# Kernel tuning notes

Measured on AMD Instinct MI355X. Metric: run time of the kernel, lower is better.

Reference implementation:

```python
import jax, jax.numpy as jnp
import numpy as np


def _next_power2(n: int) -> int:
    return 1 << (n - 1).bit_length()


def setup_inputs() -> dict:
    key = jax.random.key(0)
    k1, k2, k3 = jax.random.split(key, 3)
    N, C, W = 32, 8, 65536
    F, WW = 16, 64
    x = jax.random.normal(k1, (N, C, W), dtype=jnp.float32)
    w = jax.random.normal(k2, (F, C, WW), dtype=jnp.float32)
    b = jax.random.normal(k3, (F,), dtype=jnp.float32)
    return {"x": x, "w": w, "b": b}


def reference(x, w, b):
    # FFT-based 1D cross-correlation (valid mode), no spectral compression
    # (preserve_energy_rate=index_back=out_size=padding=None).
    N, C, W = x.shape
    F, _, WW = w.shape
    out_W = W - WW + 1
    fftsize = _next_power2(W + WW - 1)
    Xf = jnp.fft.rfft(x, fftsize)                     # (N, C, Fr) complex
    Wf = jnp.fft.rfft(w, fftsize)                     # (F, C, Fr) complex
    # correlation = irfft(X * conj(W)); sum over channels C
    prod = jnp.einsum("ncf,kcf->nkf", Xf, jnp.conj(Wf))  # (N, F, Fr)
    out = jnp.fft.irfft(prod, fftsize)[..., :out_W]      # (N, F, out_W)
    # Original code adds bias[ff] inside the channel loop -> bias added C times.
    return out + (C * b)[None, :, None]
```

## Files before the change

kernel.cpp:

```cpp
#include <hip/hip_runtime.h>
#include <stdint.h>

typedef _Float16 half8 __attribute__((ext_vector_type(8)));
typedef __fp16 fp16x2 __attribute__((ext_vector_type(2)));
typedef float f32x4 __attribute__((ext_vector_type(4)));
typedef float f32x2 __attribute__((ext_vector_type(2)));
typedef uint32_t u32x2 __attribute__((ext_vector_type(2)));

#define N_ 32
#define C_ 8
#define W_ 65536
#define F_ 16
#define OW_ 65473
#define K_ 512
#define TILE_T 1024
#define XS 1152
#define SCP 140
#define SCW 4480

__device__ __forceinline__ uint32_t funnel16(uint32_t hi, uint32_t lo) {
  return (uint32_t)((((uint64_t)hi << 32) | (uint64_t)lo) >> 16);
}

__device__ __forceinline__ uint32_t pk(float a, float b) {
  union { fp16x2 h; uint32_t u; } cv;
  cv.h = __builtin_amdgcn_cvt_pkrtz(a, b);
  return cv.u;
}

__device__ __forceinline__ uint32_t wswz(uint32_t e) {
  uint32_t ch = e >> 3;
  ch ^= (ch >> 6) & 7u;
  return (ch << 4) | ((e & 7u) << 1);
}

__device__ __forceinline__ f32x4 ldx(const float* p) {
  return *reinterpret_cast<const f32x4*>(p);
}

template<bool TAIL>
__device__ __forceinline__ void block_job(const float* __restrict__ x,
                                          const float* __restrict__ w,
                                          const float* __restrict__ b,
                                          float* __restrict__ out,
                                          char* smem, int n, int t0) {
  _Float16* wl = reinterpret_cast<_Float16*>(smem);
  _Float16* xb = reinterpret_cast<_Float16*>(smem + 16384);

  const int tid  = threadIdx.x;
  const int lane = tid & 63;
  const int wv   = tid >> 6;
  const int c15  = lane & 15;
  const int g    = lane >> 4;

  const float* xn = x + (size_t)n * (C_ * W_);

  #pragma unroll
  for (int j = 0; j < 4; ++j) {
    int e = (tid + 512 * j) * 4;
    f32x4 v = ldx(w + e);
    u32x2 p; p[0] = pk(v[0], v[1]); p[1] = pk(v[2], v[3]);
    *reinterpret_cast<u32x2*>(reinterpret_cast<char*>(wl) + wswz((uint32_t)e)) = p;
  }

  #pragma unroll
  for (int j = 0; j < 5; ++j) {
    int u = tid + 512 * j;
    if (j == 4 && u >= 2176) break;
    int ch = u / 272;
    int pos = (u - ch * 272) * 4;
    int gi = t0 + pos;
    f32x4 v;
    if (TAIL) v = (gi < W_) ? ldx(xn + (size_t)ch * W_ + gi) : (f32x4){0.f,0.f,0.f,0.f};
    else      v = ldx(xn + (size_t)ch * W_ + gi);
    u32x2 p; p[0] = pk(v[0], v[1]); p[1] = pk(v[2], v[3]);
    *reinterpret_cast<u32x2*>(reinterpret_cast<char*>(xb) + (size_t)(ch * XS + pos) * 2u) = p;
  }

  const f32x4 bv = *reinterpret_cast<const f32x4*>(b + 4 * g);

  __syncthreads();

  const int tlw = wv << 7;

  f32x4 acc[8];
  #pragma unroll
  for (int r = 0; r < 8; ++r) acc[r] = (f32x4){0.f, 0.f, 0.f, 0.f};

  union Win { half8 h[2]; uint32_t d[8]; };

  #pragma unroll
  for (int s = 0; s < 16; ++s) {
    const uint32_t we = (uint32_t)(c15 * K_ + 32 * s + 8 * g);
    const half8 wf = *reinterpret_cast<const half8*>(
                         reinterpret_cast<const char*>(wl) + wswz(we));
    const int c  = s >> 1;
    const int jb = (s & 1) * 32;
    const int A0 = tlw + 8 * c15 + jb + 8 * g;
    Win win;
    win.h[0] = *reinterpret_cast<const half8*>(xb + c * XS + A0);
    win.h[1] = *reinterpret_cast<const half8*>(xb + c * XS + A0 + 8);
    #pragma unroll
    for (int r = 0; r < 8; ++r) {
      union { uint32_t d[4]; half8 h; } fr;
      const int m = r >> 1;
      if ((r & 1) == 0) {
        fr.d[0] = win.d[m];     fr.d[1] = win.d[m + 1];
        fr.d[2] = win.d[m + 2]; fr.d[3] = win.d[m + 3];
      } else {
        fr.d[0] = funnel16(win.d[m + 1], win.d[m]);
        fr.d[1] = funnel16(win.d[m + 2], win.d[m + 1]);
        fr.d[2] = funnel16(win.d[m + 3], win.d[m + 2]);
        fr.d[3] = funnel16(win.d[m + 4], win.d[m + 3]);
      }
      acc[r] = __builtin_amdgcn_mfma_f32_16x16x32_f16(wf, fr.h, acc[r], 0, 0, 0);
    }
  }

  __syncthreads();

  float* sc = reinterpret_cast<float*>(smem + (size_t)wv * SCW);
  float* outn = out + (size_t)n * F_ * OW_;
  const int Tw  = t0 + tlw;
  const int flr = lane >> 3;
  const int k   = lane & 7;

  #pragma unroll
  for (int cb = 0; cb < 2; ++cb) {
    const int qb = 2 * cb;
    #pragma unroll
    for (int dq = 0; dq < 2; ++dq) {
      const int q  = qb + dq;
      const int fl = 2 * g + dq;
      const float bias = 8.0f * bv[q];
      f32x4 lo = { acc[0][q] + bias, acc[1][q] + bias,
                   acc[2][q] + bias, acc[3][q] + bias };
      f32x4 hi = { acc[4][q] + bias, acc[5][q] + bias,
                   acc[6][q] + bias, acc[7][q] + bias };
      *reinterpret_cast<f32x4*>(sc + fl * SCP + 8 * c15)     = lo;
      *reinterpret_cast<f32x4*>(sc + fl * SCP + 8 * c15 + 4) = hi;
    }
    const int f  = 4 * (flr >> 1) + qb + (flr & 1);
    const int tf = (16 - f) & 15;
    float* row = outn + (size_t)f * OW_ + Tw;
    #pragma unroll
    for (int j = 0; j < 7; ++j) {
      const int t = tf + 2 * k + 16 * j;
      f32x2 v = { sc[flr * SCP + t], sc[flr * SCP + t + 1] };
      if (!TAIL || Tw + t + 2 <= OW_) {
        *reinterpret_cast<f32x2*>(row + t) = v;
      } else {
        if (Tw + t     < OW_) row[t]     = v[0];
        if (Tw + t + 1 < OW_) row[t + 1] = v[1];
      }
    }
    #pragma unroll
    for (int e2 = 0; e2 < 2; ++e2) {
      const int e = k + 8 * e2;
      const int t = (e < tf) ? e : 112 + e;
      if (!TAIL || Tw + t < OW_) row[t] = sc[flr * SCP + t];
    }
  }
}

__global__ __launch_bounds__(512, 6)
void corr1d(const float* __restrict__ x, const float* __restrict__ w,
            const float* __restrict__ b, float* __restrict__ out) {
  __shared__ __align__(16) char smem[35840];

  const int n  = blockIdx.x >> 6;
  const int tt = blockIdx.x & 63;
  const int t0 = tt * TILE_T;

  if (tt < 63) block_job<false>(x, w, b, out, smem, n, t0);
  else         block_job<true >(x, w, b, out, smem, n, t0);
}

extern "C" void kernel_launch(void* const* d_in, const int* in_sizes, int n_in,
                              void* d_out, int out_size, void* d_ws, size_t ws_size,
                              hipStream_t stream) {
  (void)in_sizes; (void)n_in; (void)out_size; (void)d_ws; (void)ws_size;
  const float* x = (const float*)d_in[0];
  const float* w = (const float*)d_in[1];
  const float* b = (const float*)d_in[2];
  float* out = (float*)d_out;
  corr1d<<<dim3(32 * 64), dim3(512), 0, stream>>>(x, w, b, out);
}
```

Baseline: 50.68 us.

## Keep filter fragments in registers and loop blocks over multiple smaller tiles

Loads the fp16 weight fragments straight from global into registers once per block instead of staging them through swizzled shared memory. Blocks shrink to 256 threads and each handles four consecutive 512-sample tiles in a loop, so the weight load and conversion is amortised and shared memory use drops to about 18 KB. The cost is more registers per thread (16 half8 fragments) and an extra barrier per tile. Within each block, tile loads and compute are serialised with no prefetch, and the grid shrinks to 1024 blocks.

```diff
diff --git a/kernel.cpp b/kernel.cpp
--- a/kernel.cpp
+++ b/kernel.cpp
@@ -13,8 +13,9 @@
 #define F_ 16
 #define OW_ 65473
 #define K_ 512
-#define TILE_T 1024
-#define XS 1152
+#define TILE_T 512
+#define NT_ 4
+#define XS 576
 #define SCP 140
 #define SCW 4480
 
@@ -28,152 +29,154 @@
   return cv.u;
 }
 
-__device__ __forceinline__ uint32_t wswz(uint32_t e) {
-  uint32_t ch = e >> 3;
-  ch ^= (ch >> 6) & 7u;
-  return (ch << 4) | ((e & 7u) << 1);
-}
-
 __device__ __forceinline__ f32x4 ldx(const float* p) {
   return *reinterpret_cast<const f32x4*>(p);
 }
 
-template<bool TAIL>
+template<bool TAILB>
 __device__ __forceinline__ void block_job(const float* __restrict__ x,
                                           const float* __restrict__ w,
                                           const float* __restrict__ b,
                                           float* __restrict__ out,
-                                          char* smem, int n, int t0) {
-  _Float16* wl = reinterpret_cast<_Float16*>(smem);
-  _Float16* xb = reinterpret_cast<_Float16*>(smem + 16384);
+                                          char* smem, int n, int tb0) {
+  _Float16* xb = reinterpret_cast<_Float16*>(smem);
 
   const int tid  = threadIdx.x;
   const int lane = tid & 63;
   const int wv   = tid >> 6;
   const int c15  = lane & 15;
   const int g    = lane >> 4;
+  const int tlw  = wv << 7;
 
   const float* xn = x + (size_t)n * (C_ * W_);
+  float* outn = out + (size_t)n * F_ * OW_;
 
-  #pragma unroll
-  for (int j = 0; j < 4; ++j) {
-    int e = (tid + 512 * j) * 4;
-    f32x4 v = ldx(w + e);
-    u32x2 p; p[0] = pk(v[0], v[1]); p[1] = pk(v[2], v[3]);
-    *reinterpret_cast<u32x2*>(reinterpret_cast<char*>(wl) + wswz((uint32_t)e)) = p;
+  half8 wf[16];
+  {
+    const float* wrow = w + c15 * K_ + 8 * g;
+    #pragma unroll
+    for (int s = 0; s < 16; ++s) {
+      f32x4 a = ldx(wrow + 32 * s);
+      f32x4 c = ldx(wrow + 32 * s + 4);
+      union { uint32_t d[4]; half8 h; } u;
+      u.d[0] = pk(a[0], a[1]); u.d[1] = pk(a[2], a[3]);
+      u.d[2] = pk(c[0], c[1]); u.d[3] = pk(c[2], c[3]);
+      wf[s] = u.h;
+    }
   }
-
-  #pragma unroll
-  for (int j = 0; j < 5; ++j) {
-    int u = tid + 512 * j;
-    if (j == 4 && u >= 2176) break;
-    int ch = u / 272;
-    int pos = (u - ch * 272) * 4;
-    int gi = t0 + pos;
-    f32x4 v;
-    if (TAIL) v = (gi < W_) ? ldx(xn + (size_t)ch * W_ + gi) : (f32x4){0.f,0.f,0.f,0.f};
-    else      v = ldx(xn + (size_t)ch * W_ + gi);
-    u32x2 p; p[0] = pk(v[0], v[1]); p[1] = pk(v[2], v[3]);
-    *reinterpret_cast<u32x2*>(reinterpret_cast<char*>(xb) + (size_t)(ch * XS + pos) * 2u) = p;
-  }
-
   const f32x4 bv = *reinterpret_cast<const f32x4*>(b + 4 * g);
-
-  __syncthreads();
-
-  const int tlw = wv << 7;
-
-  f32x4 acc[8];
-  #pragma unroll
-  for (int r = 0; r < 8; ++r) acc[r] = (f32x4){0.f, 0.f, 0.f, 0.f};
 
   union Win { half8 h[2]; uint32_t d[8]; };
 
-  #pragma unroll
-  for (int s = 0; s < 16; ++s) {
-    const uint32_t we = (uint32_t)(c15 * K_ + 32 * s + 8 * g);
-    const half8 wf = *reinterpret_cast<const half8*>(
-                         reinterpret_cast<const char*>(wl) + wswz(we));
-    const int c  = s >> 1;
-    const int jb = (s & 1) * 32;
-    const int A0 = tlw + 8 * c15 + jb + 8 * g;
-    Win win;
-    win.h[0] = *reinterpret_cast<const half8*>(xb + c * XS + A0);
-    win.h[1] = *reinterpret_cast<const half8*>(xb + c * XS + A0 + 8);
+  for (int it = 0; it < NT_; ++it) {
+    const int t0 = tb0 + it * TILE_T;
+    const bool tail = TAILB && (it == NT_ - 1);
+
+    if (it) __syncthreads();
+
     #pragma unroll
-    for (int r = 0; r < 8; ++r) {
-      union { uint32_t d[4]; half8 h; } fr;
-      const int m = r >> 1;
-      if ((r & 1) == 0) {
-        fr.d[0] = win.d[m];     fr.d[1] = win.d[m + 1];
-        fr.d[2] = win.d[m + 2]; fr.d[3] = win.d[m + 3];
-      } else {
-        fr.d[0] = funnel16(win.d[m + 1], win.d[m]);
-        fr.d[1] = funnel16(win.d[m + 2], win.d[m + 1]);
-        fr.d[2] = funnel16(win.d[m + 3], win.d[m + 2]);
-        fr.d[3] = funnel16(win.d[m + 4], win.d[m + 3]);
-      }
-      acc[r] = __builtin_amdgcn_mfma_f32_16x16x32_f16(wf, fr.h, acc[r], 0, 0, 0);
+    for (int j = 0; j < 5; ++j) {
+      int u = tid + 256 * j;
+      if (j == 4 && u >= 1152) break;
+      int ch = u / 144;
+      int pos = (u - ch * 144) * 4;
+      int gi = t0 + pos;
+      f32x4 v;
+      if (tail) v = (gi < W_) ? ldx(xn + (size_t)ch * W_ + gi) : (f32x4){0.f,0.f,0.f,0.f};
+      else      v = ldx(xn + (size_t)ch * W_ + gi);
+      u32x2 p; p[0] = pk(v[0], v[1]); p[1] = pk(v[2], v[3]);
+      *reinterpret_cast<u32x2*>(reinterpret_cast<char*>(xb) +
+                                (size_t)(ch * XS + pos) * 2u) = p;
     }
-  }
 
-  __syncthreads();
+    __syncthreads();
 
-  float* sc = reinterpret_cast<float*>(smem + (size_t)wv * SCW);
-  float* outn = out + (size_t)n * F_ * OW_;
-  const int Tw  = t0 + tlw;
-  const int flr = lane >> 3;
-  const int k   = lane & 7;
+    f32x4 acc[8];
+    #pragma unroll
+    for (int r = 0; r < 8; ++r) acc[r] = (f32x4){0.f, 0.f, 0.f, 0.f};
 
-  #pragma unroll
-  for (int cb = 0; cb < 2; ++cb) {
-    const int qb = 2 * cb;
     #pragma unroll
-    for (int dq = 0; dq < 2; ++dq) {
-      const int q  = qb + dq;
-      const int fl = 2 * g + dq;
-      const float bias = 8.0f * bv[q];
-      f32x4 lo = { acc[0][q] + bias, acc[1][q] + bias,
-                   acc[2][q] + bias, acc[3][q] + bias };
-      f32x4 hi = { acc[4][q] + bias, acc[5][q] + bias,
-                   acc[6][q] + bias, acc[7][q] + bias };
-      *reinterpret_cast<f32x4*>(sc + fl * SCP + 8 * c15)     = lo;
-      *reinterpret_cast<f32x4*>(sc + fl * SCP + 8 * c15 + 4) = hi;
-    }
-    const int f  = 4 * (flr >> 1) + qb + (flr & 1);
-    const int tf = (16 - f) & 15;
-    float* row = outn + (size_t)f * OW_ + Tw;
-    #pragma unroll
-    for (int j = 0; j < 7; ++j) {
-      const int t = tf + 2 * k + 16 * j;
-      f32x2 v = { sc[flr * SCP + t], sc[flr * SCP + t + 1] };
-      if (!TAIL || Tw + t + 2 <= OW_) {
-        *reinterpret_cast<f32x2*>(row + t) = v;
-      } else {
-        if (Tw + t     < OW_) row[t]     = v[0];
-        if (Tw + t + 1 < OW_) row[t + 1] = v[1];
+    for (int s = 0; s < 16; ++s) {
+      const int c  = s >> 1;
+      const int jb = (s & 1) * 32;
+      const int A0 = tlw + 8 * c15 + jb + 8 * g;
+      Win win;
+      win.h[0] = *reinterpret_cast<const half8*>(xb + c * XS + A0);
+      win.h[1] = *reinterpret_cast<const half8*>(xb + c * XS + A0 + 8);
+      #pragma unroll
+      for (int r = 0; r < 8; ++r) {
+        union { uint32_t d[4]; half8 h; } fr;
+        const int m = r >> 1;
+        if ((r & 1) == 0) {
+          fr.d[0] = win.d[m];     fr.d[1] = win.d[m + 1];
+          fr.d[2] = win.d[m + 2]; fr.d[3] = win.d[m + 3];
+        } else {
+          fr.d[0] = funnel16(win.d[m + 1], win.d[m]);
+          fr.d[1] = funnel16(win.d[m + 2], win.d[m + 1]);
+          fr.d[2] = funnel16(win.d[m + 3], win.d[m + 2]);
+          fr.d[3] = funnel16(win.d[m + 4], win.d[m + 3]);
+        }
+        acc[r] = __builtin_amdgcn_mfma_f32_16x16x32_f16(wf[s], fr.h, acc[r], 0, 0, 0);
       }
     }
+
+    __syncthreads();
+
+    float* sc = reinterpret_cast<float*>(smem + (size_t)wv * SCW);
+    const int Tw  = t0 + tlw;
+    const int flr = lane >> 3;
+    const int k   = lane & 7;
+
     #pragma unroll
-    for (int e2 = 0; e2 < 2; ++e2) {
-      const int e = k + 8 * e2;
-      const int t = (e < tf) ? e : 112 + e;
-      if (!TAIL || Tw + t < OW_) row[t] = sc[flr * SCP + t];
+    for (int cb = 0; cb < 2; ++cb) {
+      const int qb = 2 * cb;
+      #pragma unroll
+      for (int dq = 0; dq < 2; ++dq) {
+        const int q  = qb + dq;
+        const int fl = 2 * g + dq;
+        const float bias = 8.0f * bv[q];
+        f32x4 lo = { acc[0][q] + bias, acc[1][q] + bias,
+                     acc[2][q] + bias, acc[3][q] + bias };
+        f32x4 hi = { acc[4][q] + bias, acc[5][q] + bias,
+                     acc[6][q] + bias, acc[7][q] + bias };
+        *reinterpret_cast<f32x4*>(sc + fl * SCP + 8 * c15)     = lo;
+        *reinterpret_cast<f32x4*>(sc + fl * SCP + 8 * c15 + 4) = hi;
+      }
+      const int f  = 4 * (flr >> 1) + qb + (flr & 1);
+      const int tf = (16 - f) & 15;
+      float* row = outn + (size_t)f * OW_ + Tw;
+      #pragma unroll
+      for (int j = 0; j < 7; ++j) {
+        const int t = tf + 2 * k + 16 * j;
+        f32x2 v = { sc[flr * SCP + t], sc[flr * SCP + t + 1] };
+        if (!tail || Tw + t + 2 <= OW_) {
+          *reinterpret_cast<f32x2*>(row + t) = v;
+        } else {
+          if (Tw + t     < OW_) row[t]     = v[0];
+          if (Tw + t + 1 < OW_) row[t + 1] = v[1];
+        }
+      }
+      #pragma unroll
+      for (int e2 = 0; e2 < 2; ++e2) {
+        const int e = k + 8 * e2;
+        const int t = (e < tf) ? e : 112 + e;
+        if (!tail || Tw + t < OW_) row[t] = sc[flr * SCP + t];
+      }
     }
   }
 }
 
-__global__ __launch_bounds__(512, 6)
+__global__ __launch_bounds__(256, 4)
 void corr1d(const float* __restrict__ x, const float* __restrict__ w,
             const float* __restrict__ b, float* __restrict__ out) {
-  __shared__ __align__(16) char smem[35840];
+  __shared__ __align__(16) char smem[18432];
 
-  const int n  = blockIdx.x >> 6;
-  const int tt = blockIdx.x & 63;
-  const int t0 = tt * TILE_T;
+  const int n  = blockIdx.x >> 5;
+  const int bt = blockIdx.x & 31;
+  const int tb0 = bt << 11;
 
-  if (tt < 63) block_job<false>(x, w, b, out, smem, n, t0);
-  else         block_job<true >(x, w, b, out, smem, n, t0);
+  if (bt < 31) block_job<false>(x, w, b, out, smem, n, tb0);
+  else         block_job<true >(x, w, b, out, smem, n, tb0);
 }
 
 extern "C" void kernel_launch(void* const* d_in, const int* in_sizes, int n_in,
@@ -184,5 +187,5 @@
   const float* w = (const float*)d_in[1];
   const float* b = (const float*)d_in[2];
   float* out = (float*)d_out;
-  corr1d<<<dim3(32 * 64), dim3(512), 0, stream>>>(x, w, b, out);
+  corr1d<<<dim3(32 * 32), dim3(256), 0, stream>>>(x, w, b, out);
 }
```

Result: slower. 111.5 us (+120.0%).

## Split block tile into two half-tiles with register-prefetched second load

Applied to the files above, without the earlier changes.

Each block now runs 256 threads and handles its 1024-sample span as two 512-sample sub-tiles. The second sub-tile's input is loaded into registers while the MFMA loop runs on the first, and the epilogue reuses the x buffers as scratch, so global load latency overlaps compute. The epilogue is also reworked to write four filters per wave group without the wrap-around remainder stores. In exchange there are more registers per thread, extra barriers, and half as many waves per block, which may reduce latency hiding.

```diff
diff --git a/kernel.cpp b/kernel.cpp
--- a/kernel.cpp
+++ b/kernel.cpp
@@ -7,88 +7,44 @@
 typedef float f32x2 __attribute__((ext_vector_type(2)));
 typedef uint32_t u32x2 __attribute__((ext_vector_type(2)));
 
-#define N_ 32
 #define C_ 8
 #define W_ 65536
 #define F_ 16
 #define OW_ 65473
 #define K_ 512
-#define TILE_T 1024
-#define XS 1152
+#define TILE 512
+#define XH 576
 #define SCP 140
-#define SCW 4480
 
 __device__ __forceinline__ uint32_t funnel16(uint32_t hi, uint32_t lo) {
   return (uint32_t)((((uint64_t)hi << 32) | (uint64_t)lo) >> 16);
 }
-
 __device__ __forceinline__ uint32_t pk(float a, float b) {
   union { fp16x2 h; uint32_t u; } cv;
   cv.h = __builtin_amdgcn_cvt_pkrtz(a, b);
   return cv.u;
 }
-
 __device__ __forceinline__ uint32_t wswz(uint32_t e) {
   uint32_t ch = e >> 3;
   ch ^= (ch >> 6) & 7u;
   return (ch << 4) | ((e & 7u) << 1);
 }
-
 __device__ __forceinline__ f32x4 ldx(const float* p) {
   return *reinterpret_cast<const f32x4*>(p);
 }
 
-template<bool TAIL>
-__device__ __forceinline__ void block_job(const float* __restrict__ x,
-                                          const float* __restrict__ w,
-                                          const float* __restrict__ b,
-                                          float* __restrict__ out,
-                                          char* smem, int n, int t0) {
-  _Float16* wl = reinterpret_cast<_Float16*>(smem);
-  _Float16* xb = reinterpret_cast<_Float16*>(smem + 16384);
-
-  const int tid  = threadIdx.x;
-  const int lane = tid & 63;
-  const int wv   = tid >> 6;
-  const int c15  = lane & 15;
-  const int g    = lane >> 4;
-
-  const float* xn = x + (size_t)n * (C_ * W_);
-
-  #pragma unroll
-  for (int j = 0; j < 4; ++j) {
-    int e = (tid + 512 * j) * 4;
-    f32x4 v = ldx(w + e);
-    u32x2 p; p[0] = pk(v[0], v[1]); p[1] = pk(v[2], v[3]);
-    *reinterpret_cast<u32x2*>(reinterpret_cast<char*>(wl) + wswz((uint32_t)e)) = p;
-  }
-
-  #pragma unroll
-  for (int j = 0; j < 5; ++j) {
-    int u = tid + 512 * j;
-    if (j == 4 && u >= 2176) break;
-    int ch = u / 272;
-    int pos = (u - ch * 272) * 4;
-    int gi = t0 + pos;
-    f32x4 v;
-    if (TAIL) v = (gi < W_) ? ldx(xn + (size_t)ch * W_ + gi) : (f32x4){0.f,0.f,0.f,0.f};
-    else      v = ldx(xn + (size_t)ch * W_ + gi);
-    u32x2 p; p[0] = pk(v[0], v[1]); p[1] = pk(v[2], v[3]);
-    *reinterpret_cast<u32x2*>(reinterpret_cast<char*>(xb) + (size_t)(ch * XS + pos) * 2u) = p;
-  }
-
-  const f32x4 bv = *reinterpret_cast<const f32x4*>(b + 4 * g);
-
-  __syncthreads();
-
-  const int tlw = wv << 7;
-
-  f32x4 acc[8];
-  #pragma unroll
-  for (int r = 0; r < 8; ++r) acc[r] = (f32x4){0.f, 0.f, 0.f, 0.f};
-
+__device__ __forceinline__ void wg_barrier() {
+  __builtin_amdgcn_sched_barrier(0);
+  asm volatile("s_waitcnt lgkmcnt(0)" ::: "memory");
+  __builtin_amdgcn_sched_barrier(0);
+  __builtin_amdgcn_s_barrier();
+  __builtin_amdgcn_sched_barrier(0);
+}
+
+__device__ __forceinline__ void kloop(const _Float16* __restrict__ wl,
+                                      const _Float16* __restrict__ xb,
+                                      f32x4 acc[8], int c15, int g, int tlw) {
   union Win { half8 h[2]; uint32_t d[8]; };
-
   #pragma unroll
   for (int s = 0; s < 16; ++s) {
     const uint32_t we = (uint32_t)(c15 * K_ + 32 * s + 8 * g);
@@ -98,8 +54,8 @@
     const int jb = (s & 1) * 32;
     const int A0 = tlw + 8 * c15 + jb + 8 * g;
     Win win;
-    win.h[0] = *reinterpret_cast<const half8*>(xb + c * XS + A0);
-    win.h[1] = *reinterpret_cast<const half8*>(xb + c * XS + A0 + 8);
+    win.h[0] = *reinterpret_cast<const half8*>(xb + c * XH + A0);
+    win.h[1] = *reinterpret_cast<const half8*>(xb + c * XH + A0 + 8);
     #pragma unroll
     for (int r = 0; r < 8; ++r) {
       union { uint32_t d[4]; half8 h; } fr;
@@ -116,63 +72,136 @@
       acc[r] = __builtin_amdgcn_mfma_f32_16x16x32_f16(wf, fr.h, acc[r], 0, 0, 0);
     }
   }
-
-  __syncthreads();
-
-  float* sc = reinterpret_cast<float*>(smem + (size_t)wv * SCW);
-  float* outn = out + (size_t)n * F_ * OW_;
-  const int Tw  = t0 + tlw;
-  const int flr = lane >> 3;
-  const int k   = lane & 7;
-
-  #pragma unroll
-  for (int cb = 0; cb < 2; ++cb) {
-    const int qb = 2 * cb;
-    #pragma unroll
-    for (int dq = 0; dq < 2; ++dq) {
-      const int q  = qb + dq;
-      const int fl = 2 * g + dq;
-      const float bias = 8.0f * bv[q];
-      f32x4 lo = { acc[0][q] + bias, acc[1][q] + bias,
-                   acc[2][q] + bias, acc[3][q] + bias };
-      f32x4 hi = { acc[4][q] + bias, acc[5][q] + bias,
-                   acc[6][q] + bias, acc[7][q] + bias };
-      *reinterpret_cast<f32x4*>(sc + fl * SCP + 8 * c15)     = lo;
-      *reinterpret_cast<f32x4*>(sc + fl * SCP + 8 * c15 + 4) = hi;
-    }
-    const int f  = 4 * (flr >> 1) + qb + (flr & 1);
-    const int tf = (16 - f) & 15;
+}
+
+template<bool TAILT>
+__device__ __forceinline__ void epilogue(const f32x4 acc[8], f32x4 bv,
+                                         float* __restrict__ outn,
+                                         float* __restrict__ scw,
+                                         int Tw, int lane) {
+  const int c15 = lane & 15;
+  const int g   = lane >> 4;
+  #pragma unroll
+  for (int q = 0; q < 4; ++q) {
+    const float bias = 8.0f * bv[q];
+    f32x4 lo = { acc[0][q] + bias, acc[1][q] + bias,
+                 acc[2][q] + bias, acc[3][q] + bias };
+    f32x4 hi = { acc[4][q] + bias, acc[5][q] + bias,
+                 acc[6][q] + bias, acc[7][q] + bias };
+    *reinterpret_cast<f32x4*>(scw + g * SCP + 8 * c15)     = lo;
+    *reinterpret_cast<f32x4*>(scw + g * SCP + 8 * c15 + 4) = hi;
+    const int f = 4 * g + q;
     float* row = outn + (size_t)f * OW_ + Tw;
     #pragma unroll
-    for (int j = 0; j < 7; ++j) {
-      const int t = tf + 2 * k + 16 * j;
-      f32x2 v = { sc[flr * SCP + t], sc[flr * SCP + t + 1] };
-      if (!TAIL || Tw + t + 2 <= OW_) {
+    for (int p = 0; p < 4; ++p) {
+      const int t = 2 * c15 + 32 * p;
+      f32x2 v = { scw[g * SCP + t], scw[g * SCP + t + 1] };
+      if (!TAILT || Tw + t + 2 <= OW_) {
         *reinterpret_cast<f32x2*>(row + t) = v;
       } else {
         if (Tw + t     < OW_) row[t]     = v[0];
         if (Tw + t + 1 < OW_) row[t + 1] = v[1];
       }
     }
-    #pragma unroll
-    for (int e2 = 0; e2 < 2; ++e2) {
-      const int e = k + 8 * e2;
-      const int t = (e < tf) ? e : 112 + e;
-      if (!TAIL || Tw + t < OW_) row[t] = sc[flr * SCP + t];
-    }
-  }
-}
-
-__global__ __launch_bounds__(512, 6)
+  }
+}
+
+template<bool TAILB>
+__device__ __forceinline__ void block_job(const float* __restrict__ x,
+                                          const float* __restrict__ w,
+                                          const float* __restrict__ b,
+                                          float* __restrict__ out,
+                                          char* smem, int n, int t0) {
+  _Float16* wl  = reinterpret_cast<_Float16*>(smem);
+  _Float16* xb0 = reinterpret_cast<_Float16*>(smem + 16384);
+  _Float16* xb1 = reinterpret_cast<_Float16*>(smem + 16384 + 9216);
+
+  const int tid  = threadIdx.x;
+  const int lane = tid & 63;
+  const int wv   = tid >> 6;
+  const int c15  = lane & 15;
+  const int g    = lane >> 4;
+  const int tlw  = wv << 7;
+
+  const float* xn = x + (size_t)n * (C_ * W_);
+  float* outn = out + (size_t)n * F_ * OW_;
+
+  #pragma unroll
+  for (int j = 0; j < 8; ++j) {
+    int e = (tid + 256 * j) * 4;
+    f32x4 v = ldx(w + e);
+    u32x2 p; p[0] = pk(v[0], v[1]); p[1] = pk(v[2], v[3]);
+    *reinterpret_cast<u32x2*>(reinterpret_cast<char*>(wl) + wswz((uint32_t)e)) = p;
+  }
+  #pragma unroll
+  for (int j = 0; j < 5; ++j) {
+    int u = tid + 256 * j;
+    if (j == 4 && u >= 1152) break;
+    int ch = u / 144; int pos = (u - ch * 144) * 4;
+    f32x4 v = ldx(xn + (size_t)ch * W_ + t0 + pos);
+    u32x2 p; p[0] = pk(v[0], v[1]); p[1] = pk(v[2], v[3]);
+    *reinterpret_cast<u32x2*>(reinterpret_cast<char*>(xb0) +
+                              (size_t)(ch * XH + pos) * 2u) = p;
+  }
+  f32x4 pre[5];
+  const int t1 = t0 + TILE;
+  #pragma unroll
+  for (int j = 0; j < 5; ++j) {
+    int u = tid + 256 * j;
+    if (j == 4 && u >= 1152) break;
+    int ch = u / 144; int pos = (u - ch * 144) * 4;
+    int gi = t1 + pos;
+    if (TAILB) pre[j] = (gi < W_) ? ldx(xn + (size_t)ch * W_ + gi)
+                                  : (f32x4){0.f, 0.f, 0.f, 0.f};
+    else       pre[j] = ldx(xn + (size_t)ch * W_ + gi);
+  }
+  const f32x4 bv = *reinterpret_cast<const f32x4*>(b + 4 * g);
+
+  wg_barrier();
+
+  f32x4 acc[8];
+  #pragma unroll
+  for (int r = 0; r < 8; ++r) acc[r] = (f32x4){0.f, 0.f, 0.f, 0.f};
+  kloop(wl, xb0, acc, c15, g, tlw);
+
+  #pragma unroll
+  for (int j = 0; j < 5; ++j) {
+    int u = tid + 256 * j;
+    if (j == 4 && u >= 1152) break;
+    int ch = u / 144; int pos = (u - ch * 144) * 4;
+    u32x2 p; p[0] = pk(pre[j][0], pre[j][1]); p[1] = pk(pre[j][2], pre[j][3]);
+    *reinterpret_cast<u32x2*>(reinterpret_cast<char*>(xb1) +
+                              (size_t)(ch * XH + pos) * 2u) = p;
+  }
+
+  wg_barrier();
+
+  epilogue<false>(acc, bv, outn,
+                  reinterpret_cast<float*>(reinterpret_cast<char*>(xb0) + wv * 2240),
+                  t0 + tlw, lane);
+
+  f32x4 acc2[8];
+  #pragma unroll
+  for (int r = 0; r < 8; ++r) acc2[r] = (f32x4){0.f, 0.f, 0.f, 0.f};
+  kloop(wl, xb1, acc2, c15, g, tlw);
+
+  wg_barrier();
+
+  epilogue<TAILB>(acc2, bv, outn,
+                  reinterpret_cast<float*>(reinterpret_cast<char*>(xb1) + wv * 2240),
+                  t1 + tlw, lane);
+}
+
+__global__ __launch_bounds__(256, 4)
 void corr1d(const float* __restrict__ x, const float* __restrict__ w,
             const float* __restrict__ b, float* __restrict__ out) {
-  __shared__ __align__(16) char smem[35840];
+  __shared__ __align__(16) char smem[16384 + 2 * 9216];
 
   const int n  = blockIdx.x >> 6;
-  const int tt = blockIdx.x & 63;
-  const int t0 = tt * TILE_T;
-
-  if (tt < 63) block_job<false>(x, w, b, out, smem, n, t0);
+  const int bt = blockIdx.x & 63;
+  const int t0 = bt << 10;
+
+  if (bt < 63) block_job<false>(x, w, b, out, smem, n, t0);
   else         block_job<true >(x, w, b, out, smem, n, t0);
 }
 
@@ -184,5 +213,5 @@
   const float* w = (const float*)d_in[1];
   const float* b = (const float*)d_in[2];
   float* out = (float*)d_out;
-  corr1d<<<dim3(32 * 64), dim3(512), 0, stream>>>(x, w, b, out);
-}
+  corr1d<<<dim3(32 * 64), dim3(256), 0, stream>>>(x, w, b, out);
+}
```

New measurement: 61.40 us. 1.21x slower.

## Double output tile per block and store first half directly from registers

Applied to the files above, without the earlier changes.

Each block now covers 2048 output positions instead of 1024. It loads the weights once and runs two MFMA passes over a larger staged input window, which halves the grid and the per-block weight staging and barrier overhead. The first pass writes results straight from accumulator registers with unaligned vector stores. Only the second pass uses the LDS transpose epilogue, and it is guarded by a lighter lgkmcnt barrier. LDS use rises to about 52KB per block, which may reduce occupancy, and the direct register stores are less coalesced.

```diff
diff --git a/kernel.cpp b/kernel.cpp
--- a/kernel.cpp
+++ b/kernel.cpp
@@ -7,88 +7,45 @@
 typedef float f32x2 __attribute__((ext_vector_type(2)));
 typedef uint32_t u32x2 __attribute__((ext_vector_type(2)));
 
-#define N_ 32
 #define C_ 8
 #define W_ 65536
 #define F_ 16
 #define OW_ 65473
 #define K_ 512
-#define TILE_T 1024
-#define XS 1152
+#define TILE 2048
+#define XH2 2176
 #define SCP 140
 #define SCW 4480
 
 __device__ __forceinline__ uint32_t funnel16(uint32_t hi, uint32_t lo) {
   return (uint32_t)((((uint64_t)hi << 32) | (uint64_t)lo) >> 16);
 }
-
 __device__ __forceinline__ uint32_t pk(float a, float b) {
   union { fp16x2 h; uint32_t u; } cv;
   cv.h = __builtin_amdgcn_cvt_pkrtz(a, b);
   return cv.u;
 }
-
 __device__ __forceinline__ uint32_t wswz(uint32_t e) {
   uint32_t ch = e >> 3;
   ch ^= (ch >> 6) & 7u;
   return (ch << 4) | ((e & 7u) << 1);
 }
-
 __device__ __forceinline__ f32x4 ldx(const float* p) {
   return *reinterpret_cast<const f32x4*>(p);
 }
 
-template<bool TAIL>
-__device__ __forceinline__ void block_job(const float* __restrict__ x,
-                                          const float* __restrict__ w,
-                                          const float* __restrict__ b,
-                                          float* __restrict__ out,
-                                          char* smem, int n, int t0) {
-  _Float16* wl = reinterpret_cast<_Float16*>(smem);
-  _Float16* xb = reinterpret_cast<_Float16*>(smem + 16384);
-
-  const int tid  = threadIdx.x;
-  const int lane = tid & 63;
-  const int wv   = tid >> 6;
-  const int c15  = lane & 15;
-  const int g    = lane >> 4;
-
-  const float* xn = x + (size_t)n * (C_ * W_);
-
-  #pragma unroll
-  for (int j = 0; j < 4; ++j) {
-    int e = (tid + 512 * j) * 4;
-    f32x4 v = ldx(w + e);
-    u32x2 p; p[0] = pk(v[0], v[1]); p[1] = pk(v[2], v[3]);
-    *reinterpret_cast<u32x2*>(reinterpret_cast<char*>(wl) + wswz((uint32_t)e)) = p;
-  }
-
-  #pragma unroll
-  for (int j = 0; j < 5; ++j) {
-    int u = tid + 512 * j;
-    if (j == 4 && u >= 2176) break;
-    int ch = u / 272;
-    int pos = (u - ch * 272) * 4;
-    int gi = t0 + pos;
-    f32x4 v;
-    if (TAIL) v = (gi < W_) ? ldx(xn + (size_t)ch * W_ + gi) : (f32x4){0.f,0.f,0.f,0.f};
-    else      v = ldx(xn + (size_t)ch * W_ + gi);
-    u32x2 p; p[0] = pk(v[0], v[1]); p[1] = pk(v[2], v[3]);
-    *reinterpret_cast<u32x2*>(reinterpret_cast<char*>(xb) + (size_t)(ch * XS + pos) * 2u) = p;
-  }
-
-  const f32x4 bv = *reinterpret_cast<const f32x4*>(b + 4 * g);
-
-  __syncthreads();
-
-  const int tlw = wv << 7;
-
-  f32x4 acc[8];
-  #pragma unroll
-  for (int r = 0; r < 8; ++r) acc[r] = (f32x4){0.f, 0.f, 0.f, 0.f};
-
+__device__ __forceinline__ void wg_barrier_lgkm() {
+  __builtin_amdgcn_sched_barrier(0);
+  asm volatile("s_waitcnt lgkmcnt(0)" ::: "memory");
+  __builtin_amdgcn_sched_barrier(0);
+  __builtin_amdgcn_s_barrier();
+  __builtin_amdgcn_sched_barrier(0);
+}
+
+__device__ __forceinline__ void kloop(const _Float16* __restrict__ wl,
+                                      const _Float16* __restrict__ xb,
+                                      f32x4 acc[8], int c15, int g, int off) {
   union Win { half8 h[2]; uint32_t d[8]; };
-
   #pragma unroll
   for (int s = 0; s < 16; ++s) {
     const uint32_t we = (uint32_t)(c15 * K_ + 32 * s + 8 * g);
@@ -96,10 +53,10 @@
                          reinterpret_cast<const char*>(wl) + wswz(we));
     const int c  = s >> 1;
     const int jb = (s & 1) * 32;
-    const int A0 = tlw + 8 * c15 + jb + 8 * g;
+    const int A0 = off + 8 * c15 + jb + 8 * g;
     Win win;
-    win.h[0] = *reinterpret_cast<const half8*>(xb + c * XS + A0);
-    win.h[1] = *reinterpret_cast<const half8*>(xb + c * XS + A0 + 8);
+    win.h[0] = *reinterpret_cast<const half8*>(xb + c * XH2 + A0);
+    win.h[1] = *reinterpret_cast<const half8*>(xb + c * XH2 + A0 + 8);
     #pragma unroll
     for (int r = 0; r < 8; ++r) {
       union { uint32_t d[4]; half8 h; } fr;
@@ -116,15 +73,45 @@
       acc[r] = __builtin_amdgcn_mfma_f32_16x16x32_f16(wf, fr.h, acc[r], 0, 0, 0);
     }
   }
-
-  __syncthreads();
-
-  float* sc = reinterpret_cast<float*>(smem + (size_t)wv * SCW);
-  float* outn = out + (size_t)n * F_ * OW_;
-  const int Tw  = t0 + tlw;
+}
+
+__device__ __forceinline__ void epi_reg(const f32x4 acc[8], f32x4 bv,
+                                        float* __restrict__ outn,
+                                        int T, int g) {
+  #pragma unroll
+  for (int q = 0; q < 4; ++q) {
+    const float bias = 8.0f * bv[q];
+    float sv[8];
+    #pragma unroll
+    for (int j = 0; j < 8; ++j) sv[j] = acc[j][q] + bias;
+    float* row = outn + (size_t)(4 * g + q) * OW_ + T;
+    if (q == 0) {
+      *reinterpret_cast<f32x4*>(row)     = (f32x4){sv[0], sv[1], sv[2], sv[3]};
+      *reinterpret_cast<f32x4*>(row + 4) = (f32x4){sv[4], sv[5], sv[6], sv[7]};
+    } else if (q == 2) {
+      *reinterpret_cast<f32x2*>(row)     = (f32x2){sv[0], sv[1]};
+      *reinterpret_cast<f32x2*>(row + 2) = (f32x2){sv[2], sv[3]};
+      *reinterpret_cast<f32x2*>(row + 4) = (f32x2){sv[4], sv[5]};
+      *reinterpret_cast<f32x2*>(row + 6) = (f32x2){sv[6], sv[7]};
+    } else {
+      row[0] = sv[0];
+      *reinterpret_cast<f32x2*>(row + 1) = (f32x2){sv[1], sv[2]};
+      *reinterpret_cast<f32x2*>(row + 3) = (f32x2){sv[3], sv[4]};
+      *reinterpret_cast<f32x2*>(row + 5) = (f32x2){sv[5], sv[6]};
+      row[7] = sv[7];
+    }
+  }
+}
+
+template<bool TAILT>
+__device__ __forceinline__ void epi_lds(const f32x4 acc[8], f32x4 bv,
+                                        float* __restrict__ outn,
+                                        float* __restrict__ scw,
+                                        int Tw, int lane) {
+  const int c15 = lane & 15;
+  const int g   = lane >> 4;
   const int flr = lane >> 3;
   const int k   = lane & 7;
-
   #pragma unroll
   for (int cb = 0; cb < 2; ++cb) {
     const int qb = 2 * cb;
@@ -137,8 +124,8 @@
                    acc[2][q] + bias, acc[3][q] + bias };
       f32x4 hi = { acc[4][q] + bias, acc[5][q] + bias,
                    acc[6][q] + bias, acc[7][q] + bias };
-      *reinterpret_cast<f32x4*>(sc + fl * SCP + 8 * c15)     = lo;
-      *reinterpret_cast<f32x4*>(sc + fl * SCP + 8 * c15 + 4) = hi;
+      *reinterpret_cast<f32x4*>(scw + fl * SCP + 8 * c15)     = lo;
+      *reinterpret_cast<f32x4*>(scw + fl * SCP + 8 * c15 + 4) = hi;
     }
     const int f  = 4 * (flr >> 1) + qb + (flr & 1);
     const int tf = (16 - f) & 15;
@@ -146,8 +133,8 @@
     #pragma unroll
     for (int j = 0; j < 7; ++j) {
       const int t = tf + 2 * k + 16 * j;
-      f32x2 v = { sc[flr * SCP + t], sc[flr * SCP + t + 1] };
-      if (!TAIL || Tw + t + 2 <= OW_) {
+      f32x2 v = { scw[flr * SCP + t], scw[flr * SCP + t + 1] };
+      if (!TAILT || Tw + t + 2 <= OW_) {
         *reinterpret_cast<f32x2*>(row + t) = v;
       } else {
         if (Tw + t     < OW_) row[t]     = v[0];
@@ -158,21 +145,84 @@
     for (int e2 = 0; e2 < 2; ++e2) {
       const int e = k + 8 * e2;
       const int t = (e < tf) ? e : 112 + e;
-      if (!TAIL || Tw + t < OW_) row[t] = sc[flr * SCP + t];
-    }
-  }
+      if (!TAILT || Tw + t < OW_) row[t] = scw[flr * SCP + t];
+    }
+  }
+}
+
+template<bool TAILB>
+__device__ __forceinline__ void block_job(const float* __restrict__ x,
+                                          const float* __restrict__ w,
+                                          const float* __restrict__ b,
+                                          float* __restrict__ out,
+                                          char* smem, int n, int t0) {
+  _Float16* wl = reinterpret_cast<_Float16*>(smem);
+  _Float16* xb = reinterpret_cast<_Float16*>(smem + 16384);
+  char* scbase = smem + 16384;
+
+  const int tid  = threadIdx.x;
+  const int lane = tid & 63;
+  const int wv   = tid >> 6;
+  const int c15  = lane & 15;
+  const int g    = lane >> 4;
+  const int tlw  = wv << 7;
+
+  const float* xn = x + (size_t)n * (C_ * W_);
+  float* outn = out + (size_t)n * F_ * OW_;
+
+  #pragma unroll
+  for (int j = 0; j < 4; ++j) {
+    int e = (tid + 512 * j) * 4;
+    f32x4 v = ldx(w + e);
+    u32x2 p; p[0] = pk(v[0], v[1]); p[1] = pk(v[2], v[3]);
+    *reinterpret_cast<u32x2*>(reinterpret_cast<char*>(wl) + wswz((uint32_t)e)) = p;
+  }
+  #pragma unroll
+  for (int j = 0; j < 9; ++j) {
+    int u = tid + 512 * j;
+    if (j == 8 && u >= 4224) break;
+    int ch = u / 528;
+    int pos = (u - ch * 528) * 4;
+    int gi = t0 + pos;
+    f32x4 v;
+    if (TAILB) v = (gi < W_) ? ldx(xn + (size_t)ch * W_ + gi) : (f32x4){0.f,0.f,0.f,0.f};
+    else       v = ldx(xn + (size_t)ch * W_ + gi);
+    u32x2 p; p[0] = pk(v[0], v[1]); p[1] = pk(v[2], v[3]);
+    *reinterpret_cast<u32x2*>(reinterpret_cast<char*>(xb) +
+                              (size_t)(ch * XH2 + pos) * 2u) = p;
+  }
+
+  const f32x4 bv = *reinterpret_cast<const f32x4*>(b + 4 * g);
+
+  __syncthreads();
+
+  f32x4 acc[8];
+  #pragma unroll
+  for (int r = 0; r < 8; ++r) acc[r] = (f32x4){0.f, 0.f, 0.f, 0.f};
+  kloop(wl, xb, acc, c15, g, tlw);
+  epi_reg(acc, bv, outn, t0 + tlw + 8 * c15, g);
+
+  #pragma unroll
+  for (int r = 0; r < 8; ++r) acc[r] = (f32x4){0.f, 0.f, 0.f, 0.f};
+  kloop(wl, xb, acc, c15, g, tlw + 1024);
+
+  wg_barrier_lgkm();
+
+  epi_lds<TAILB>(acc, bv, outn,
+                 reinterpret_cast<float*>(scbase + (size_t)wv * SCW),
+                 t0 + 1024 + tlw, lane);
 }
 
 __global__ __launch_bounds__(512, 6)
 void corr1d(const float* __restrict__ x, const float* __restrict__ w,
             const float* __restrict__ b, float* __restrict__ out) {
-  __shared__ __align__(16) char smem[35840];
-
-  const int n  = blockIdx.x >> 6;
-  const int tt = blockIdx.x & 63;
-  const int t0 = tt * TILE_T;
-
-  if (tt < 63) block_job<false>(x, w, b, out, smem, n, t0);
+  __shared__ __align__(16) char smem[16384 + 35840];
+
+  const int n  = blockIdx.x >> 5;
+  const int bt = blockIdx.x & 31;
+  const int t0 = bt << 11;
+
+  if (bt < 31) block_job<false>(x, w, b, out, smem, n, t0);
   else         block_job<true >(x, w, b, out, smem, n, t0);
 }
 
@@ -184,5 +234,5 @@
   const float* w = (const float*)d_in[1];
   const float* b = (const float*)d_in[2];
   float* out = (float*)d_out;
-  corr1d<<<dim3(32 * 64), dim3(512), 0, stream>>>(x, w, b, out);
-}
+  corr1d<<<dim3(32 * 32), dim3(512), 0, stream>>>(x, w, b, out);
+}
```

After: 202.7 us. 4x slower.
